# Kernel optimization log

Measured on AMD Instinct MI355X. Metric: run time of the kernel, lower is better.

The kernel has to match this reference:

```python
import jax, jax.numpy as jnp
import numpy as np

B, T, H, V = 32, 256, 1024, 256


def setup_inputs() -> dict:
    key = jax.random.key(0)
    ks = jax.random.split(key, 12)
    xavier = float(np.sqrt(6.0 / (H + V)))
    inp = {
        "x": jax.random.randint(ks[0], (B, T), 0, V, dtype=jnp.int64),
        "targets": jax.random.randint(ks[1], (B, T), 0, V, dtype=jnp.int64),
        "h0": jnp.zeros((B, H), jnp.float32),
        "c0": jnp.zeros((B, H), jnp.float32),
        "h1": jnp.zeros((B, H), jnp.float32),
        "c1": jnp.zeros((B, H), jnp.float32),
        # learned params
        "emb": jax.random.normal(ks[2], (V, H), jnp.float32) * 0.05,
        "W_ih0": jax.random.normal(ks[3], (H, 4 * H), jnp.float32) / np.sqrt(H),
        "W_hh0": jax.random.normal(ks[4], (H, 4 * H), jnp.float32) / np.sqrt(H),
        "b0": jnp.zeros((4 * H,), jnp.float32),
        "W_ih1": jax.random.normal(ks[5], (H, 4 * H), jnp.float32) / np.sqrt(H),
        "W_hh1": jax.random.normal(ks[6], (H, 4 * H), jnp.float32) / np.sqrt(H),
        "b1": jnp.zeros((4 * H,), jnp.float32),
        "W_out": jax.random.uniform(ks[7], (H, V), jnp.float32, -xavier, xavier),
        "b_out": jnp.zeros((V,), jnp.float32),
    }
    return inp


def _lstm_cell(h, c, inp, W_ih, W_hh, b):
    # gates: [B, 4H] -> i, f, g, o
    z = inp @ W_ih + h @ W_hh + b
    i, f, g, o = jnp.split(z, 4, axis=-1)
    c_new = jax.nn.sigmoid(f) * c + jax.nn.sigmoid(i) * jnp.tanh(g)
    h_new = jax.nn.sigmoid(o) * jnp.tanh(c_new)
    return h_new, c_new


def reference(x, targets, h0, c0, h1, c1, emb, W_ih0, W_hh0, b0,
              W_ih1, W_hh1, b1, W_out, b_out):
    # Teacher-forcing branch: embed targets, feed embedding at every step.
    embeddings = emb[targets]            # [B, T, H]
    e_seq = jnp.swapaxes(embeddings, 0, 1)  # [T, B, H] for scan over time

    def step(carry, e_t):
        (h0, c0), (h1, c1) = carry
        h0, c0 = _lstm_cell(h0, c0, e_t, W_ih0, W_hh0, b0)
        h1, c1 = _lstm_cell(h1, c1, h0, W_ih1, W_hh1, b1)
        logit = h1 @ W_out + b_out       # [B, V]
        return ((h0, c0), (h1, c1)), logit

    carry0 = ((h0, c0), (h1, c1))
    carry_f, logits_tbv = jax.lax.scan(step, carry0, e_seq)
    logits = jnp.swapaxes(logits_tbv, 0, 1)  # [B, T, V]
    (h0f, c0f), (h1f, c1f) = carry_f
    return logits, h0f, c0f, h1f, c1f
```

## Files before the change

### kernel.cpp

```cpp
#include <hip/hip_runtime.h>
#include <cstdint>


typedef float    f32x4 __attribute__((ext_vector_type(4)));
typedef short    s16x8 __attribute__((ext_vector_type(8)));
typedef unsigned u32x4 __attribute__((ext_vector_type(4)));

#define DEV __device__ __forceinline__

DEV unsigned short f2bf(float x){
  unsigned u = __builtin_bit_cast(unsigned, x);
  unsigned r = (u + 0x7fffu + ((u >> 16) & 1u)) >> 16;
  return (unsigned short)r;
}
DEV float bf2f(unsigned short b){ return __builtin_bit_cast(float, ((unsigned)b) << 16); }

DEV s16x8 ld16(const void* p){ return *(const s16x8*)p; }

DEV f32x4 MF(s16x8 a, s16x8 b, f32x4 c){
  return __builtin_amdgcn_mfma_f32_16x16x32_bf16(a, b, c, 0, 0, 0);
}

#define LDC(dst, ptr)  asm volatile("global_load_dwordx4 %0, %1, off sc0 sc1" : "=v"(dst) : "v"(ptr))
#define LDP(dst, ptr)  asm volatile("global_load_dwordx4 %0, %1, off"         : "=v"(dst) : "v"(ptr))
#define WAITVM(n) do { asm volatile("s_waitcnt vmcnt(" #n ")" ::: "memory"); \
                       __builtin_amdgcn_sched_barrier(0); } while (0)
#define CFENCE()  asm volatile("" ::: "memory")
#define TRIPLE(Cmn, Ahm, Alm, Bhn, Bln) do { \
    Cmn = MF(Ahm, Bhn, Cmn); Cmn = MF(Ahm, Bln, Cmn); Cmn = MF(Alm, Bhn, Cmn); } while (0)

DEV void st16c(void* p, u32x4 v){
  asm volatile("global_store_dwordx4 %0, %1, off sc0 sc1" :: "v"(p), "v"(v) : "memory");
}
DEV void set_flag(int* p, int v){
  __hip_atomic_store(p, v, __ATOMIC_RELAXED, __HIP_MEMORY_SCOPE_AGENT);
}
DEV void poll2(const int* f, int lane, int target){
  const int* p0 = f + lane * 8;
  const int* p1 = f + (64 + lane) * 8;
  for (;;) {
    int a = __hip_atomic_load(p0, __ATOMIC_RELAXED, __HIP_MEMORY_SCOPE_AGENT);
    int b = __hip_atomic_load(p1, __ATOMIC_RELAXED, __HIP_MEMORY_SCOPE_AGENT);
    if (__all((a >= target) && (b >= target))) break;
    __builtin_amdgcn_s_sleep(1);
  }
  CFENCE();
}
DEV char* h0slot(char* wa0, char* s0, char* hi, int s){
  return (s == 0) ? s0 : ((s <= 128) ? wa0 + ((size_t)(s - 1) << 17)
                                     : hi  + ((size_t)(s - 129) << 17));
}

__global__ void prep_wfrag(const float* __restrict__ W0, const float* __restrict__ W1,
                           const float* __restrict__ W2, const float* __restrict__ W3,
                           char* D0, char* D1, char* D2, char* D3) {
  int gid = blockIdx.x * 256 + threadIdx.x;
  int lane = gid & 63, ks = (gid >> 6) & 31, jb = (gid >> 11) & 255, mat = gid >> 19;
  const float* S = (mat == 0) ? W0 : (mat == 1) ? W1 : (mat == 2) ? W2 : W3;
  char* D = (mat == 0) ? D0 : (mat == 1) ? D1 : (mat == 2) ? D2 : D3;
  int jp = jb * 16 + (lane & 15), u = jp >> 2, g = jp & 3;
  int kb = ks * 32 + (lane >> 4) * 8;
  s16x8 vh, vl;
  #pragma unroll
  for (int i = 0; i < 8; ++i) {
    float x = S[(kb + i) * 4096 + g * 1024 + u];
    unsigned short h = f2bf(x);
    vh[i] = (short)h;
    vl[i] = (short)f2bf(x - bf2f(h));
  }
  *(s16x8*)(D + (((jb * 2 + 0) * 32 + ks) << 10) + lane * 16) = vh;
  *(s16x8*)(D + (((jb * 2 + 1) * 32 + ks) << 10) + lane * 16) = vl;
}

__global__ void prep_bfrag(const float* __restrict__ emb, const float* __restrict__ Wout,
                           char* Demb, char* Dwout) {
  int gid = blockIdx.x * 256 + threadIdx.x;
  int lane = gid & 63, ks = (gid >> 6) & 31, vb = (gid >> 11) & 15, which = gid >> 15;
  int v = vb * 16 + (lane & 15), kb = ks * 32 + (lane >> 4) * 8;
  s16x8 vh, vl;
  #pragma unroll
  for (int i = 0; i < 8; ++i) {
    float x = which ? Wout[(kb + i) * 256 + v] : emb[v * 1024 + kb + i];
    unsigned short h = f2bf(x);
    vh[i] = (short)h;
    vl[i] = (short)f2bf(x - bf2f(h));
  }
  char* D = which ? Dwout : Demb;
  *(s16x8*)(D + (((vb * 2 + 0) * 32 + ks) << 10) + lane * 16) = vh;
  *(s16x8*)(D + (((vb * 2 + 1) * 32 + ks) << 10) + lane * 16) = vl;
}

__global__ void prep_hinit(const float* __restrict__ h0, const float* __restrict__ h1,
                           char* h0s0, char* h1f) {
  int gid = blockIdx.x * 256 + threadIdx.x;
  int lane = gid & 63, ks = (gid >> 6) & 31, nt = (gid >> 11) & 1, which = gid >> 12;
  const float* S = which ? h1 : h0;
  char* D = which ? h1f : h0s0;
  int b = nt * 16 + (lane & 15), kb = ks * 32 + (lane >> 4) * 8;
  s16x8 vh, vl;
  #pragma unroll
  for (int i = 0; i < 8; ++i) {
    float x = S[b * 1024 + kb + i];
    unsigned short h = f2bf(x);
    vh[i] = (short)h;
    vl[i] = (short)f2bf(x - bf2f(h));
  }
  *(s16x8*)(D + (((0 * 2 + nt) * 32 + ks) << 10) + lane * 16) = vh;
  *(s16x8*)(D + (((1 * 2 + nt) * 32 + ks) << 10) + lane * 16) = vl;
}

__global__ void prep_misc(const float* __restrict__ b1, float* b1i, int* f0a, int* f1a) {
  int i = blockIdx.x * 256 + threadIdx.x;
  if (i < 4096) b1i[i] = b1[(i & 3) * 1024 + (i >> 2)];
  if (i < 1024) { f0a[i] = -1; f1a[i] = -1; }
}

__global__ __launch_bounds__(256, 1) void lstm_persist(
    const int* __restrict__ tgt,
    const float* __restrict__ c0_in, const float* __restrict__ c1_in,
    const float* __restrict__ b0, const float* __restrict__ b_out,
    char* __restrict__ WA0, const char* __restrict__ WA1, const char* __restrict__ WA2,
    const char* __restrict__ WAi0, const char* __restrict__ WoutB, const char* __restrict__ embB,
    float* __restrict__ E0, const float* __restrict__ b1i,
    char* __restrict__ h0s0, char* __restrict__ h0hi, char* __restrict__ h1frag,
    int* __restrict__ f0, int* __restrict__ f1,
    float* __restrict__ out)
{
  extern __shared__ char smem[];
  constexpr int PART = 131072;
  constexpr int RP   = 131072 + 16384;
  const int tid = threadIdx.x, lane = tid & 63, wv = tid >> 6;
  const int wg = blockIdx.x;
  const bool isL0 = (wg < 128);
  const int wgl = isL0 ? wg : (wg - 128);
  const int l15 = lane & 15, l4 = lane >> 4;
  const int mi_e = wv >> 1, nt_e = wv & 1;

  __builtin_amdgcn_fence(__ATOMIC_ACQUIRE, "agent");

  if (isL0) {
    u32x4 tmp[8];
    for (int blk = 0; blk < 4; ++blk) {
      #pragma unroll
      for (int q = 0; q < 8; ++q) {
        int idx = tid + (blk * 8 + q) * 256;
        int l16 = idx & 63, ks = (idx >> 6) & 31, mi = (idx >> 11) & 1, part = idx >> 12;
        LDC(tmp[q], WA0 + ((((wgl * 2 + mi) * 2 + part) * 32 + ks) << 10) + l16 * 16);
      }
      WAITVM(0);
      #pragma unroll
      for (int q = 0; q < 8; ++q) {
        int idx = tid + (blk * 8 + q) * 256;
        int l16 = idx & 63, ks = (idx >> 6) & 31, mi = (idx >> 11) & 1, part = idx >> 12;
        *(u32x4*)(smem + (((part * 2 + mi) * 32 + ks) << 10) + l16 * 16) = tmp[q];
      }
    }
  } else {
    for (int idx = tid; idx < 8192; idx += 256) {
      int l16 = idx & 63, ks = (idx >> 6) & 31, mi = (idx >> 11) & 1, mat = idx >> 12;
      const char* W = mat ? WA2 : WA1;
      u32x4 v = *(const u32x4*)(W + ((((wgl * 2 + mi) * 2 + 0) * 32 + ks) << 10) + l16 * 16);
      *(u32x4*)(smem + (((mat * 2 + mi) * 32 + ks) << 10) + l16 * 16) = v;
    }
  }

  if (isL0) {
    f32x4 C[2][4];
    #pragma unroll
    for (int a = 0; a < 2; ++a)
      #pragma unroll
      for (int b = 0; b < 4; ++b) C[a][b] = 0.0f;
    for (int ks = 0; ks < 32; ++ks) {
      s16x8 Ah0, Ah1, Al0, Al1;
      LDC(Ah0, WAi0 + ((((wgl * 2 + 0) * 2 + 0) * 32 + ks) << 10) + lane * 16);
      LDC(Ah1, WAi0 + ((((wgl * 2 + 1) * 2 + 0) * 32 + ks) << 10) + lane * 16);
      LDC(Al0, WAi0 + ((((wgl * 2 + 0) * 2 + 1) * 32 + ks) << 10) + lane * 16);
      LDC(Al1, WAi0 + ((((wgl * 2 + 1) * 2 + 1) * 32 + ks) << 10) + lane * 16);
      WAITVM(0);
      #pragma unroll
      for (int v4 = 0; v4 < 4; ++v4) {
        int vb = wv * 4 + v4;
        s16x8 Bh = ld16(embB + (((vb * 2 + 0) * 32 + ks) << 10) + lane * 16);
        s16x8 Bl = ld16(embB + (((vb * 2 + 1) * 32 + ks) << 10) + lane * 16);
        TRIPLE(C[0][v4], Ah0, Al0, Bh, Bl);
        TRIPLE(C[1][v4], Ah1, Al1, Bh, Bl);
      }
    }
    #pragma unroll
    for (int mi = 0; mi < 2; ++mi) {
      int jb4 = wgl * 32 + mi * 16 + l4 * 4;
      int u = jb4 >> 2;
      f32x4 bb;
      #pragma unroll
      for (int r = 0; r < 4; ++r) bb[r] = b0[r * 1024 + u];
      #pragma unroll
      for (int v4 = 0; v4 < 4; ++v4) {
        int v = (wv * 4 + v4) * 16 + l15;
        *(f32x4*)(E0 + v * 4096 + jb4) = C[mi][v4] + bb;
      }
    }
  }

  float cst;
  {
    const float* cs = isL0 ? c0_in : c1_in;
    cst = cs[(nt_e * 16 + l15) * 1024 + wgl * 8 + mi_e * 4 + l4];
  }
  f32x4 b1z = {0.f, 0.f, 0.f, 0.f};
  if (!isL0) b1z = *(const f32x4*)(b1i + wgl * 32 + mi_e * 16 + (l4 << 2));

  __syncthreads();
  if (tid == 0) set_flag((isL0 ? f0 : f1) + wgl * 8, 0);

  for (int t = 0; t < 256; ++t) {
    const int s = t + 1;
    f32x4 C[2][2];
    #pragma unroll
    for (int a = 0; a < 2; ++a)
      #pragma unroll
      for (int b = 0; b < 2; ++b) C[a][b] = 0.0f;

    f32x4 e0v = {0.f, 0.f, 0.f, 0.f};

    if (isL0) {
      int tv = tgt[(nt_e * 16 + l15) * 256 + t];
      e0v = *(const f32x4*)(E0 + (size_t)tv * 4096 + wgl * 32 + mi_e * 16 + (l4 << 2));
      poll2(f0, lane, t);
      const char* Bb = h0slot(WA0, h0s0, h0hi, t);
      const int ksb = wv * 8;
      s16x8 P[3][4];
      #pragma unroll
      for (int d = 0; d < 2; ++d)
        #pragma unroll
        for (int q = 0; q < 4; ++q) LDP(P[d][q], Bb + ((q * 32 + ksb + d) << 10) + lane * 16);
      #pragma unroll
      for (int i = 0; i < 8; ++i) {
        const int ks = ksb + i;
        if (i < 6) {
          #pragma unroll
          for (int q = 0; q < 4; ++q) LDP(P[(i + 2) % 3][q], Bb + ((q * 32 + ks + 2) << 10) + lane * 16);
        }
        s16x8 Ah0 = ld16(smem + ((0 * 32 + ks) << 10) + lane * 16);
        s16x8 Ah1 = ld16(smem + ((1 * 32 + ks) << 10) + lane * 16);
        s16x8 Al0 = ld16(smem + ((2 * 32 + ks) << 10) + lane * 16);
        s16x8 Al1 = ld16(smem + ((3 * 32 + ks) << 10) + lane * 16);
        if (i < 6) { WAITVM(8); } else if (i == 6) { WAITVM(4); } else { WAITVM(0); }
        TRIPLE(C[0][0], Ah0, Al0, P[i % 3][0], P[i % 3][2]);
        TRIPLE(C[0][1], Ah0, Al0, P[i % 3][1], P[i % 3][3]);
        TRIPLE(C[1][0], Ah1, Al1, P[i % 3][0], P[i % 3][2]);
        TRIPLE(C[1][1], Ah1, Al1, P[i % 3][1], P[i % 3][3]);
      }
    } else {
      const int mat = (wv < 2) ? 1 : 0;
      if (wv < 2) poll2(f1, lane, t); else poll2(f0, lane, s);
      const char* Bb  = (wv < 2) ? (h1frag + (size_t)t * 131072)
                                 : h0slot(WA0, h0s0, h0hi, s);
      const char* ALb = (wv < 2) ? WA2 : WA1;
      const int ksb = (wv & 1) * 16;
      s16x8 P[3][4], AL[3][2];
      #pragma unroll
      for (int d = 0; d < 2; ++d) {
        #pragma unroll
        for (int q = 0; q < 4; ++q) LDP(P[d][q], Bb + ((q * 32 + ksb + d) << 10) + lane * 16);
        LDP(AL[d][0], ALb + ((((wgl * 2 + 0) * 2 + 1) * 32 + ksb + d) << 10) + lane * 16);
        LDP(AL[d][1], ALb + ((((wgl * 2 + 1) * 2 + 1) * 32 + ksb + d) << 10) + lane * 16);
      }
      #pragma unroll
      for (int i = 0; i < 16; ++i) {
        const int ks = ksb + i;
        if (i < 14) {
          #pragma unroll
          for (int q = 0; q < 4; ++q) LDP(P[(i + 2) % 3][q], Bb + ((q * 32 + ks + 2) << 10) + lane * 16);
          LDP(AL[(i + 2) % 3][0], ALb + ((((wgl * 2 + 0) * 2 + 1) * 32 + ks + 2) << 10) + lane * 16);
          LDP(AL[(i + 2) % 3][1], ALb + ((((wgl * 2 + 1) * 2 + 1) * 32 + ks + 2) << 10) + lane * 16);
        }
        s16x8 Ah0 = ld16(smem + (((mat * 2 + 0) * 32 + ks) << 10) + lane * 16);
        s16x8 Ah1 = ld16(smem + (((mat * 2 + 1) * 32 + ks) << 10) + lane * 16);
        if (i < 14) { WAITVM(12); } else if (i == 14) { WAITVM(6); } else { WAITVM(0); }
        TRIPLE(C[0][0], Ah0, AL[i % 3][0], P[i % 3][0], P[i % 3][2]);
        TRIPLE(C[0][1], Ah0, AL[i % 3][0], P[i % 3][1], P[i % 3][3]);
        TRIPLE(C[1][0], Ah1, AL[i % 3][1], P[i % 3][0], P[i % 3][2]);
        TRIPLE(C[1][1], Ah1, AL[i % 3][1], P[i % 3][1], P[i % 3][3]);
      }
    }

    #pragma unroll
    for (int mi = 0; mi < 2; ++mi)
      #pragma unroll
      for (int nt = 0; nt < 2; ++nt)
        *(f32x4*)(smem + PART + ((wv * 4 + mi * 2 + nt) << 10) + lane * 16) = C[mi][nt];
    __syncthreads();

    {
      f32x4 z = *(const f32x4*)(smem + PART + ((0 * 4 + wv) << 10) + lane * 16);
      #pragma unroll
      for (int w = 1; w < 4; ++w)
        z += *(const f32x4*)(smem + PART + ((w * 4 + wv) << 10) + lane * 16);
      z += isL0 ? e0v : b1z;
      float ig = 1.f / (1.f + __expf(-z[0]));
      float fg = 1.f / (1.f + __expf(-z[1]));
      float og = 1.f / (1.f + __expf(-z[3]));
      float cn = fg * cst + ig * tanhf(z[2]);
      float hn = og * tanhf(cn);
      cst = cn;
      unsigned short hb = f2bf(hn);
      unsigned short lb = f2bf(hn - bf2f(hb));
      *(short*)(smem + RP + ((0 + nt_e) * 16 + l15) * 16 + (mi_e * 4 + l4) * 2) = (short)hb;
      *(short*)(smem + RP + ((2 + nt_e) * 16 + l15) * 16 + (mi_e * 4 + l4) * 2) = (short)lb;
      if (t == 255) {
        int u = wgl * 8 + mi_e * 4 + l4, b = nt_e * 16 + l15;
        int off = isL0 ? 0 : 65536;
        out[2097152 + off + b * 1024 + u] = hn;
        out[2097152 + off + 32768 + b * 1024 + u] = cn;
      }
    }
    __syncthreads();

    if (wv == 0) {
      char* hd = isL0 ? h0slot(WA0, h0s0, h0hi, s)
                      : (h1frag + (size_t)s * 131072);
      u32x4 v = *(const u32x4*)(smem + RP + lane * 16);
      char* dst = hd + (((lane >> 4) * 32 + (wgl >> 2)) << 10) + ((wgl & 3) * 16 + l15) * 16;
      st16c(dst, v);
      asm volatile("s_waitcnt vmcnt(0)" ::: "memory");
      if (lane == 0) set_flag((isL0 ? f0 : f1) + wgl * 8, s);
    }
  }

  {
    const int tp = isL0 ? (128 + wgl) : wgl;
    poll2(f1, lane, tp + 1);
    const char* A = h1frag + (size_t)(tp + 1) * 131072;
    f32x4 C[2][4];
    #pragma unroll
    for (int a = 0; a < 2; ++a)
      #pragma unroll
      for (int b = 0; b < 4; ++b) C[a][b] = 0.0f;
    s16x8 QA[4], QB[4];
    #pragma unroll
    for (int q = 0; q < 4; ++q) LDP(QA[q], A + ((q * 32 + 0) << 10) + lane * 16);
    for (int kk = 0; kk < 16; ++kk) {
      const int ks = kk * 2;
      #pragma unroll
      for (int q = 0; q < 4; ++q) LDP(QB[q], A + ((q * 32 + ks + 1) << 10) + lane * 16);
      asm volatile("s_waitcnt vmcnt(4)" ::: "memory");
      __builtin_amdgcn_sched_barrier(0);
      #pragma unroll
      for (int v4 = 0; v4 < 4; ++v4) {
        int vb = wv * 4 + v4;
        s16x8 Bh = ld16(WoutB + (((vb * 2 + 0) * 32 + ks) << 10) + lane * 16);
        s16x8 Bl = ld16(WoutB + (((vb * 2 + 1) * 32 + ks) << 10) + lane * 16);
        C[0][v4] = MF(QA[0], Bh, C[0][v4]); C[0][v4] = MF(QA[0], Bl, C[0][v4]); C[0][v4] = MF(QA[2], Bh, C[0][v4]);
        C[1][v4] = MF(QA[1], Bh, C[1][v4]); C[1][v4] = MF(QA[1], Bl, C[1][v4]); C[1][v4] = MF(QA[3], Bh, C[1][v4]);
      }
      if (kk < 15) {
        #pragma unroll
        for (int q = 0; q < 4; ++q) LDP(QA[q], A + ((q * 32 + ks + 2) << 10) + lane * 16);
        asm volatile("s_waitcnt vmcnt(4)" ::: "memory");
      } else {
        asm volatile("s_waitcnt vmcnt(0)" ::: "memory");
      }
      __builtin_amdgcn_sched_barrier(0);
      #pragma unroll
      for (int v4 = 0; v4 < 4; ++v4) {
        int vb = wv * 4 + v4;
        s16x8 Bh = ld16(WoutB + (((vb * 2 + 0) * 32 + ks + 1) << 10) + lane * 16);
        s16x8 Bl = ld16(WoutB + (((vb * 2 + 1) * 32 + ks + 1) << 10) + lane * 16);
        C[0][v4] = MF(QB[0], Bh, C[0][v4]); C[0][v4] = MF(QB[0], Bl, C[0][v4]); C[0][v4] = MF(QB[2], Bh, C[0][v4]);
        C[1][v4] = MF(QB[1], Bh, C[1][v4]); C[1][v4] = MF(QB[1], Bl, C[1][v4]); C[1][v4] = MF(QB[3], Bh, C[1][v4]);
      }
    }
    #pragma unroll
    for (int nt = 0; nt < 2; ++nt)
      #pragma unroll
      for (int v4 = 0; v4 < 4; ++v4) {
        int v = (wv * 4 + v4) * 16 + l15;
        float bo = b_out[v];
        #pragma unroll
        for (int r = 0; r < 4; ++r) {
          int b = nt * 16 + l4 * 4 + r;
          out[((size_t)b * 256 + tp) * 256 + v] = C[nt][v4][r] + bo;
        }
      }
  }
}

extern "C" void kernel_launch(void* const* d_in, const int* in_sizes, int n_in,
                              void* d_out, int out_size, void* d_ws, size_t ws_size,
                              hipStream_t stream) {
  const int*   targets = (const int*)d_in[1];
  const float* h0_in   = (const float*)d_in[2];
  const float* c0_in   = (const float*)d_in[3];
  const float* h1_in   = (const float*)d_in[4];
  const float* c1_in   = (const float*)d_in[5];
  const float* emb     = (const float*)d_in[6];
  const float* W_ih0   = (const float*)d_in[7];
  const float* W_hh0   = (const float*)d_in[8];
  const float* b0      = (const float*)d_in[9];
  const float* W_ih1   = (const float*)d_in[10];
  const float* W_hh1   = (const float*)d_in[11];
  const float* b1      = (const float*)d_in[12];
  const float* W_out   = (const float*)d_in[13];
  const float* b_out   = (const float*)d_in[14];
  float* out = (float*)d_out;

  char* ws = (char*)d_ws;
  char*  WA0    = ws;
  char*  WA1    = ws + 16777216;
  char*  WA2    = ws + 33554432;
  char*  WoutB  = ws + 50331648;
  char*  embB   = ws + 51380224;
  float* E0     = (float*)(ws + 52428800);
  float* b1i    = (float*)(ws + 56623104);
  int*   f0     = (int*)(ws + 56639488);
  int*   f1     = (int*)(ws + 56643584);
  char*  h0s0   = ws + 56647680;
  char*  h0hi   = ws + 56778752;
  char*  h1frag = ws + 73555968;
  char*  WAi0   = h1frag + 16777216;

  prep_misc <<<18,   256, 0, stream>>>(b1, b1i, f0, f1);
  prep_wfrag<<<8192, 256, 0, stream>>>(W_hh0, W_ih1, W_hh1, W_ih0, WA0, WA1, WA2, WAi0);
  prep_bfrag<<<256,  256, 0, stream>>>(emb, W_out, embB, WoutB);
  prep_hinit<<<32,   256, 0, stream>>>(h0_in, h1_in, h0s0, h1frag);

  hipFuncSetAttribute(reinterpret_cast<const void*>(lstm_persist),
                      hipFuncAttributeMaxDynamicSharedMemorySize, 148480);
  lstm_persist<<<256, 256, 148480, stream>>>(
      targets, c0_in, c1_in, b0, b_out,
      WA0, WA1, WA2, WAi0, WoutB, embB,
      E0, b1i, h0s0, h0hi, h1frag, f0, f1, out);
}
```

Before: 1.873 ms.

## Split layer-1 step into precomputed input GEMM and recurrent-only critical path

Layer-1 workgroups now compute the h0-to-gates partial (W_ih1 · h0[t+1]) one step ahead, after publishing h1, so the recurrent step's critical path contains only the W_hh1 · h1 half-GEMM. All four waves split the K dimension of each half-GEMM instead of two waves per matrix. The aim is to take the wait on layer-0 output off the layer-1 dependency chain. The change also adds extra syncthreads per step, tunes poll sleep intervals, and swaps which workgroups handle the early versus late logits projection.

```diff
diff --git a/kernel.cpp b/kernel.cpp
--- a/kernel.cpp
+++ b/kernel.cpp
@@ -35,20 +35,50 @@
 DEV void set_flag(int* p, int v){
   __hip_atomic_store(p, v, __ATOMIC_RELAXED, __HIP_MEMORY_SCOPE_AGENT);
 }
-DEV void poll2(const int* f, int lane, int target){
+template<int SLP>
+DEV void pollT(const int* f, int lane, int target){
   const int* p0 = f + lane * 8;
   const int* p1 = f + (64 + lane) * 8;
   for (;;) {
     int a = __hip_atomic_load(p0, __ATOMIC_RELAXED, __HIP_MEMORY_SCOPE_AGENT);
     int b = __hip_atomic_load(p1, __ATOMIC_RELAXED, __HIP_MEMORY_SCOPE_AGENT);
     if (__all((a >= target) && (b >= target))) break;
-    __builtin_amdgcn_s_sleep(1);
+    __builtin_amdgcn_s_sleep(SLP);
   }
   CFENCE();
 }
 DEV char* h0slot(char* wa0, char* s0, char* hi, int s){
   return (s == 0) ? s0 : ((s <= 128) ? wa0 + ((size_t)(s - 1) << 17)
                                      : hi  + ((size_t)(s - 129) << 17));
+}
+
+DEV void halfgemm8(const char* smemMat, const char* ALb, const char* Bb,
+                   int wgl, int ksb, int lane, f32x4 (&C)[2][2]) {
+  s16x8 P[3][4], AL[3][2];
+  #pragma unroll
+  for (int d = 0; d < 2; ++d) {
+    #pragma unroll
+    for (int q = 0; q < 4; ++q) LDP(P[d][q], Bb + ((q * 32 + ksb + d) << 10) + lane * 16);
+    LDP(AL[d][0], ALb + ((((wgl * 2 + 0) * 2 + 1) * 32 + ksb + d) << 10) + lane * 16);
+    LDP(AL[d][1], ALb + ((((wgl * 2 + 1) * 2 + 1) * 32 + ksb + d) << 10) + lane * 16);
+  }
+  #pragma unroll
+  for (int i = 0; i < 8; ++i) {
+    const int ks = ksb + i;
+    if (i < 6) {
+      #pragma unroll
+      for (int q = 0; q < 4; ++q) LDP(P[(i + 2) % 3][q], Bb + ((q * 32 + ks + 2) << 10) + lane * 16);
+      LDP(AL[(i + 2) % 3][0], ALb + ((((wgl * 2 + 0) * 2 + 1) * 32 + ks + 2) << 10) + lane * 16);
+      LDP(AL[(i + 2) % 3][1], ALb + ((((wgl * 2 + 1) * 2 + 1) * 32 + ks + 2) << 10) + lane * 16);
+    }
+    s16x8 Ah0 = ld16(smemMat + ((0 * 32 + ks) << 10) + lane * 16);
+    s16x8 Ah1 = ld16(smemMat + ((1 * 32 + ks) << 10) + lane * 16);
+    if (i < 6) { WAITVM(12); } else if (i == 6) { WAITVM(6); } else { WAITVM(0); }
+    TRIPLE(C[0][0], Ah0, AL[i % 3][0], P[i % 3][0], P[i % 3][2]);
+    TRIPLE(C[0][1], Ah0, AL[i % 3][0], P[i % 3][1], P[i % 3][3]);
+    TRIPLE(C[1][0], Ah1, AL[i % 3][1], P[i % 3][0], P[i % 3][2]);
+    TRIPLE(C[1][1], Ah1, AL[i % 3][1], P[i % 3][1], P[i % 3][3]);
+  }
 }
 
 __global__ void prep_wfrag(const float* __restrict__ W0, const float* __restrict__ W1,
@@ -212,20 +242,18 @@
   __syncthreads();
   if (tid == 0) set_flag((isL0 ? f0 : f1) + wgl * 8, 0);
 
-  for (int t = 0; t < 256; ++t) {
-    const int s = t + 1;
-    f32x4 C[2][2];
-    #pragma unroll
-    for (int a = 0; a < 2; ++a)
-      #pragma unroll
-      for (int b = 0; b < 2; ++b) C[a][b] = 0.0f;
-
-    f32x4 e0v = {0.f, 0.f, 0.f, 0.f};
-
-    if (isL0) {
+  if (isL0) {
+    for (int t = 0; t < 256; ++t) {
+      const int s = t + 1;
+      f32x4 C[2][2];
+      #pragma unroll
+      for (int a = 0; a < 2; ++a)
+        #pragma unroll
+        for (int b = 0; b < 2; ++b) C[a][b] = 0.0f;
+
       int tv = tgt[(nt_e * 16 + l15) * 256 + t];
-      e0v = *(const f32x4*)(E0 + (size_t)tv * 4096 + wgl * 32 + mi_e * 16 + (l4 << 2));
-      poll2(f0, lane, t);
+      f32x4 e0v = *(const f32x4*)(E0 + (size_t)tv * 4096 + wgl * 32 + mi_e * 16 + (l4 << 2));
+      pollT<1>(f0, lane, t);
       const char* Bb = h0slot(WA0, h0s0, h0hi, t);
       const int ksb = wv * 8;
       s16x8 P[3][4];
@@ -250,86 +278,147 @@
         TRIPLE(C[1][0], Ah1, Al1, P[i % 3][0], P[i % 3][2]);
         TRIPLE(C[1][1], Ah1, Al1, P[i % 3][1], P[i % 3][3]);
       }
-    } else {
-      const int mat = (wv < 2) ? 1 : 0;
-      if (wv < 2) poll2(f1, lane, t); else poll2(f0, lane, s);
-      const char* Bb  = (wv < 2) ? (h1frag + (size_t)t * 131072)
-                                 : h0slot(WA0, h0s0, h0hi, s);
-      const char* ALb = (wv < 2) ? WA2 : WA1;
-      const int ksb = (wv & 1) * 16;
-      s16x8 P[3][4], AL[3][2];
-      #pragma unroll
-      for (int d = 0; d < 2; ++d) {
-        #pragma unroll
-        for (int q = 0; q < 4; ++q) LDP(P[d][q], Bb + ((q * 32 + ksb + d) << 10) + lane * 16);
-        LDP(AL[d][0], ALb + ((((wgl * 2 + 0) * 2 + 1) * 32 + ksb + d) << 10) + lane * 16);
-        LDP(AL[d][1], ALb + ((((wgl * 2 + 1) * 2 + 1) * 32 + ksb + d) << 10) + lane * 16);
-      }
-      #pragma unroll
-      for (int i = 0; i < 16; ++i) {
-        const int ks = ksb + i;
-        if (i < 14) {
+
+      #pragma unroll
+      for (int mi = 0; mi < 2; ++mi)
+        #pragma unroll
+        for (int nt = 0; nt < 2; ++nt)
+          *(f32x4*)(smem + PART + ((wv * 4 + mi * 2 + nt) << 10) + lane * 16) = C[mi][nt];
+      __syncthreads();
+
+      {
+        f32x4 z = *(const f32x4*)(smem + PART + ((0 * 4 + wv) << 10) + lane * 16);
+        #pragma unroll
+        for (int w = 1; w < 4; ++w)
+          z += *(const f32x4*)(smem + PART + ((w * 4 + wv) << 10) + lane * 16);
+        z += e0v;
+        float ig = 1.f / (1.f + __expf(-z[0]));
+        float fg = 1.f / (1.f + __expf(-z[1]));
+        float og = 1.f / (1.f + __expf(-z[3]));
+        float cn = fg * cst + ig * tanhf(z[2]);
+        float hn = og * tanhf(cn);
+        cst = cn;
+        unsigned short hb = f2bf(hn);
+        unsigned short lb = f2bf(hn - bf2f(hb));
+        *(short*)(smem + RP + ((0 + nt_e) * 16 + l15) * 16 + (mi_e * 4 + l4) * 2) = (short)hb;
+        *(short*)(smem + RP + ((2 + nt_e) * 16 + l15) * 16 + (mi_e * 4 + l4) * 2) = (short)lb;
+        if (t == 255) {
+          int u = wgl * 8 + mi_e * 4 + l4, b = nt_e * 16 + l15;
+          out[2097152 + b * 1024 + u] = hn;
+          out[2097152 + 32768 + b * 1024 + u] = cn;
+        }
+      }
+      __syncthreads();
+
+      if (wv == 0) {
+        char* hd = h0slot(WA0, h0s0, h0hi, s);
+        u32x4 v = *(const u32x4*)(smem + RP + lane * 16);
+        char* dst = hd + (((lane >> 4) * 32 + (wgl >> 2)) << 10) + ((wgl & 3) * 16 + l15) * 16;
+        st16c(dst, v);
+        asm volatile("s_waitcnt vmcnt(0)" ::: "memory");
+        if (lane == 0) set_flag(f0 + wgl * 8, s);
+      }
+    }
+  } else {
+    f32x4 zpre;
+    {
+      pollT<2>(f0, lane, 1);
+      f32x4 C2[2][2];
+      #pragma unroll
+      for (int a = 0; a < 2; ++a)
+        #pragma unroll
+        for (int b = 0; b < 2; ++b) C2[a][b] = 0.0f;
+      halfgemm8(smem, WA1, h0slot(WA0, h0s0, h0hi, 1), wgl, wv * 8, lane, C2);
+      #pragma unroll
+      for (int mi = 0; mi < 2; ++mi)
+        #pragma unroll
+        for (int nt = 0; nt < 2; ++nt)
+          *(f32x4*)(smem + PART + ((wv * 4 + mi * 2 + nt) << 10) + lane * 16) = C2[mi][nt];
+      __syncthreads();
+      zpre = *(const f32x4*)(smem + PART + ((0 * 4 + wv) << 10) + lane * 16);
+      #pragma unroll
+      for (int w = 1; w < 4; ++w)
+        zpre += *(const f32x4*)(smem + PART + ((w * 4 + wv) << 10) + lane * 16);
+      __syncthreads();
+    }
+
+    for (int t = 0; t < 256; ++t) {
+      const int s = t + 1;
+      f32x4 C[2][2];
+      #pragma unroll
+      for (int a = 0; a < 2; ++a)
+        #pragma unroll
+        for (int b = 0; b < 2; ++b) C[a][b] = 0.0f;
+
+      pollT<1>(f1, lane, t);
+      halfgemm8(smem + 65536, WA2, h1frag + (size_t)t * 131072, wgl, wv * 8, lane, C);
+
+      #pragma unroll
+      for (int mi = 0; mi < 2; ++mi)
+        #pragma unroll
+        for (int nt = 0; nt < 2; ++nt)
+          *(f32x4*)(smem + PART + ((wv * 4 + mi * 2 + nt) << 10) + lane * 16) = C[mi][nt];
+      __syncthreads();
+
+      {
+        f32x4 z = *(const f32x4*)(smem + PART + ((0 * 4 + wv) << 10) + lane * 16);
+        #pragma unroll
+        for (int w = 1; w < 4; ++w)
+          z += *(const f32x4*)(smem + PART + ((w * 4 + wv) << 10) + lane * 16);
+        z += zpre + b1z;
+        float ig = 1.f / (1.f + __expf(-z[0]));
+        float fg = 1.f / (1.f + __expf(-z[1]));
+        float og = 1.f / (1.f + __expf(-z[3]));
+        float cn = fg * cst + ig * tanhf(z[2]);
+        float hn = og * tanhf(cn);
+        cst = cn;
+        unsigned short hb = f2bf(hn);
+        unsigned short lb = f2bf(hn - bf2f(hb));
+        *(short*)(smem + RP + ((0 + nt_e) * 16 + l15) * 16 + (mi_e * 4 + l4) * 2) = (short)hb;
+        *(short*)(smem + RP + ((2 + nt_e) * 16 + l15) * 16 + (mi_e * 4 + l4) * 2) = (short)lb;
+        if (t == 255) {
+          int u = wgl * 8 + mi_e * 4 + l4, b = nt_e * 16 + l15;
+          out[2097152 + 65536 + b * 1024 + u] = hn;
+          out[2097152 + 65536 + 32768 + b * 1024 + u] = cn;
+        }
+      }
+      __syncthreads();
+
+      if (wv == 0) {
+        char* hd = h1frag + (size_t)s * 131072;
+        u32x4 v = *(const u32x4*)(smem + RP + lane * 16);
+        char* dst = hd + (((lane >> 4) * 32 + (wgl >> 2)) << 10) + ((wgl & 3) * 16 + l15) * 16;
+        st16c(dst, v);
+        asm volatile("s_waitcnt vmcnt(0)" ::: "memory");
+        if (lane == 0) set_flag(f1 + wgl * 8, s);
+      }
+
+      if (t < 255) {
+        pollT<2>(f0, lane, t + 2);
+        f32x4 C2[2][2];
+        #pragma unroll
+        for (int a = 0; a < 2; ++a)
           #pragma unroll
-          for (int q = 0; q < 4; ++q) LDP(P[(i + 2) % 3][q], Bb + ((q * 32 + ks + 2) << 10) + lane * 16);
-          LDP(AL[(i + 2) % 3][0], ALb + ((((wgl * 2 + 0) * 2 + 1) * 32 + ks + 2) << 10) + lane * 16);
-          LDP(AL[(i + 2) % 3][1], ALb + ((((wgl * 2 + 1) * 2 + 1) * 32 + ks + 2) << 10) + lane * 16);
-        }
-        s16x8 Ah0 = ld16(smem + (((mat * 2 + 0) * 32 + ks) << 10) + lane * 16);
-        s16x8 Ah1 = ld16(smem + (((mat * 2 + 1) * 32 + ks) << 10) + lane * 16);
-        if (i < 14) { WAITVM(12); } else if (i == 14) { WAITVM(6); } else { WAITVM(0); }
-        TRIPLE(C[0][0], Ah0, AL[i % 3][0], P[i % 3][0], P[i % 3][2]);
-        TRIPLE(C[0][1], Ah0, AL[i % 3][0], P[i % 3][1], P[i % 3][3]);
-        TRIPLE(C[1][0], Ah1, AL[i % 3][1], P[i % 3][0], P[i % 3][2]);
-        TRIPLE(C[1][1], Ah1, AL[i % 3][1], P[i % 3][1], P[i % 3][3]);
-      }
-    }
-
-    #pragma unroll
-    for (int mi = 0; mi < 2; ++mi)
-      #pragma unroll
-      for (int nt = 0; nt < 2; ++nt)
-        *(f32x4*)(smem + PART + ((wv * 4 + mi * 2 + nt) << 10) + lane * 16) = C[mi][nt];
-    __syncthreads();
-
-    {
-      f32x4 z = *(const f32x4*)(smem + PART + ((0 * 4 + wv) << 10) + lane * 16);
-      #pragma unroll
-      for (int w = 1; w < 4; ++w)
-        z += *(const f32x4*)(smem + PART + ((w * 4 + wv) << 10) + lane * 16);
-      z += isL0 ? e0v : b1z;
-      float ig = 1.f / (1.f + __expf(-z[0]));
-      float fg = 1.f / (1.f + __expf(-z[1]));
-      float og = 1.f / (1.f + __expf(-z[3]));
-      float cn = fg * cst + ig * tanhf(z[2]);
-      float hn = og * tanhf(cn);
-      cst = cn;
-      unsigned short hb = f2bf(hn);
-      unsigned short lb = f2bf(hn - bf2f(hb));
-      *(short*)(smem + RP + ((0 + nt_e) * 16 + l15) * 16 + (mi_e * 4 + l4) * 2) = (short)hb;
-      *(short*)(smem + RP + ((2 + nt_e) * 16 + l15) * 16 + (mi_e * 4 + l4) * 2) = (short)lb;
-      if (t == 255) {
-        int u = wgl * 8 + mi_e * 4 + l4, b = nt_e * 16 + l15;
-        int off = isL0 ? 0 : 65536;
-        out[2097152 + off + b * 1024 + u] = hn;
-        out[2097152 + off + 32768 + b * 1024 + u] = cn;
-      }
-    }
-    __syncthreads();
-
-    if (wv == 0) {
-      char* hd = isL0 ? h0slot(WA0, h0s0, h0hi, s)
-                      : (h1frag + (size_t)s * 131072);
-      u32x4 v = *(const u32x4*)(smem + RP + lane * 16);
-      char* dst = hd + (((lane >> 4) * 32 + (wgl >> 2)) << 10) + ((wgl & 3) * 16 + l15) * 16;
-      st16c(dst, v);
-      asm volatile("s_waitcnt vmcnt(0)" ::: "memory");
-      if (lane == 0) set_flag((isL0 ? f0 : f1) + wgl * 8, s);
+          for (int b = 0; b < 2; ++b) C2[a][b] = 0.0f;
+        halfgemm8(smem, WA1, h0slot(WA0, h0s0, h0hi, t + 2), wgl, wv * 8, lane, C2);
+        #pragma unroll
+        for (int mi = 0; mi < 2; ++mi)
+          #pragma unroll
+          for (int nt = 0; nt < 2; ++nt)
+            *(f32x4*)(smem + PART + ((wv * 4 + mi * 2 + nt) << 10) + lane * 16) = C2[mi][nt];
+        __syncthreads();
+        zpre = *(const f32x4*)(smem + PART + ((0 * 4 + wv) << 10) + lane * 16);
+        #pragma unroll
+        for (int w = 1; w < 4; ++w)
+          zpre += *(const f32x4*)(smem + PART + ((w * 4 + wv) << 10) + lane * 16);
+        __syncthreads();
+      }
     }
   }
 
   {
-    const int tp = isL0 ? (128 + wgl) : wgl;
-    poll2(f1, lane, tp + 1);
+    const int tp = isL0 ? wgl : (128 + wgl);
+    pollT<32>(f1, lane, tp + 1);
     const char* A = h1frag + (size_t)(tp + 1) * 131072;
     f32x4 C[2][4];
     #pragma unroll
```

Measured after the change: 1.729 ms, median of 2. 7.7% less time.
